# Kernel optimization log

Hardware: AMD Instinct MI355X
Metric: run time of the kernel (lower is better)

## Reference

```python
import jax, jax.numpy as jnp
import numpy as np

B = 65536      # batch
DIM = 32       # flow dimension
NH = 24        # hidden width of each per-dim MLP
PARITY = False # order = reversed(range(dim)) when parity is False
NEG_SLOPE = 0.2


def _causal_mask(dim, dtype):
    # mask[k, j] = 1 if j <= k ; stacked layer k corresponds to torch layer i=k+1
    # which sees x[:, :i] = columns 0..k
    return (jnp.arange(dim)[None, :] <= jnp.arange(dim - 1)[:, None]).astype(dtype)


def setup_inputs() -> dict:
    key = jax.random.key(0)
    ks = jax.random.split(key, 10)
    s = 0.1
    x = jax.random.normal(ks[0], (B, DIM), jnp.float32)
    p0 = jax.random.normal(ks[1], (2,), jnp.float32) * s          # LeafParam(2)
    W1 = jax.random.normal(ks[2], (DIM - 1, NH, DIM), jnp.float32) * s
    W1 = W1 * _causal_mask(DIM, jnp.float32)[:, None, :]          # zero padded cols j > k
    b1 = jax.random.normal(ks[3], (DIM - 1, NH), jnp.float32) * s
    W2 = jax.random.normal(ks[4], (DIM - 1, NH, NH), jnp.float32) * s
    b2 = jax.random.normal(ks[5], (DIM - 1, NH), jnp.float32) * s
    W3 = jax.random.normal(ks[6], (DIM - 1, NH, NH), jnp.float32) * s
    b3 = jax.random.normal(ks[7], (DIM - 1, NH), jnp.float32) * s
    W4 = jax.random.normal(ks[8], (DIM - 1, 2, NH), jnp.float32) * s
    b4 = jax.random.normal(ks[9], (DIM - 1, 2), jnp.float32) * s
    return {"x": x, "p0": p0, "W1": W1, "b1": b1, "W2": W2, "b2": b2,
            "W3": W3, "b3": b3, "W4": W4, "b4": b4}


def reference(x, p0, W1, b1, W2, b2, W3, b3, W4, b4):
    # SlowMAF.forward: per-dim MLP(x[:, :i]) -> (s, t); z[:, order[i]] = x[:, i]*exp(s)+t
    # All dim-1 tiny MLPs are fused into stacked batched GEMMs; the growing slice
    # x[:, :i] is realized via a causal mask on the first-layer weights (same math).
    Bsz, dim = x.shape
    lrelu = lambda h: jnp.where(h > 0, h, NEG_SLOPE * h)  # LeakyReLU(0.2)
    W1m = W1 * _causal_mask(dim, x.dtype)[:, None, :]
    h = lrelu(jnp.einsum('bd,khd->bkh', x, W1m) + b1)      # (B, dim-1, NH)
    h = lrelu(jnp.einsum('bkh,kHh->bkH', h, W2) + b2)
    h = lrelu(jnp.einsum('bkh,kHh->bkH', h, W3) + b3)
    st = jnp.einsum('bkh,koh->bko', h, W4) + b4            # (B, dim-1, 2)
    st0 = jnp.broadcast_to(p0[None, None, :], (Bsz, 1, 2)) # LeafParam for dim 0
    st_all = jnp.concatenate([st0, st], axis=1)            # (B, dim, 2)
    s = st_all[..., 0]
    t = st_all[..., 1]
    vals = x * jnp.exp(s) + t                              # (B, dim)
    order = jnp.arange(dim) if PARITY else jnp.arange(dim)[::-1]
    z = jnp.zeros_like(x).at[:, order].set(vals)
    log_det = jnp.sum(s, axis=1)                           # (B,)
    return z, log_det
```

## Files before the change

kernel.cpp:

```cpp
#include <hip/hip_runtime.h>

#define BATCH 65536
#define DIM 32
#define NEG 0.2f

typedef short    sfrag8 __attribute__((ext_vector_type(8)));
typedef _Float16 hfrag8 __attribute__((ext_vector_type(8)));
typedef _Float16 h2     __attribute__((ext_vector_type(2)));
typedef float    f32x16 __attribute__((ext_vector_type(16)));
typedef unsigned u32x4  __attribute__((ext_vector_type(4)));

__device__ __forceinline__ short f2h(float v) {
    _Float16 h = (_Float16)v;
    return __builtin_bit_cast(short, h);
}

__device__ __forceinline__ h2 cvt2h(float a, float b) {
    return __builtin_bit_cast(h2, __builtin_amdgcn_cvt_pkrtz(a, b));
}

__device__ __forceinline__ unsigned pack2h(float a, float b) {
    return __builtin_bit_cast(unsigned, __builtin_amdgcn_cvt_pkrtz(a, b));
}

__device__ float frag_elem(int k, int f, int r, int h, int j,
    const float* W1, const float* b1, const float* W2, const float* b2,
    const float* W3, const float* b3, const float* W4, const float* b4)
{
    if (f == 0) return (r < 24) ? W1[k*768 + r*32 + 8*h + j] : 0.f;
    if (f == 1) {
        if (r >= 24) return 0.f;
        int c = 16 + 8*h + j;
        if (c == 31) return b1[k*24 + r];
        return W1[k*768 + r*32 + c];
    }
    const float* W; const float* bb; int R;
    if (f < 4)      { W = W2 + k*576; bb = b2 + k*24; R = 24; }
    else if (f < 6) { W = W3 + k*576; bb = b3 + k*24; R = 24; }
    else            { W = W4 + k*48;  bb = b4 + k*2;  R = 2;  }
    if (r >= R) return 0.f;
    if ((f & 1) == 0) {
        int feat = j + 4*h + (j >= 4 ? 4 : 0);
        return W[r*24 + feat];
    } else {
        if (j < 4)            return W[r*24 + 16 + 4*h + j];
        if (j == 4 && h == 0) return bb[r];
        return 0.f;
    }
}

__global__ __launch_bounds__(256) void prep_frags(
    const float* __restrict__ W1, const float* __restrict__ b1,
    const float* __restrict__ W2, const float* __restrict__ b2,
    const float* __restrict__ W3, const float* __restrict__ b3,
    const float* __restrict__ W4, const float* __restrict__ b4,
    short* __restrict__ wsf)
{
    int t = blockIdx.x * 256 + threadIdx.x;
    int lane = t & 63, f = (t >> 6) & 7, k = t >> 9;
    int r = lane & 31, h = lane >> 5;
    sfrag8 o;
    #pragma unroll
    for (int j = 0; j < 8; j++)
        o[j] = f2h(frag_elem(k, f, r, h, j, W1, b1, W2, b2, W3, b3, W4, b4));
    *(sfrag8*)(wsf + (size_t)t * 8) = o;
}

__device__ __forceinline__ void transition(const f32x16 a, unsigned c1,
                                           hfrag8& blo, hfrag8& bhi)
{
    const h2 s02 = {(_Float16)0.2f, (_Float16)0.2f};
    unsigned P[6];
    #pragma unroll
    for (int g = 0; g < 6; g++) {
        h2 v = cvt2h(a[2*g], a[2*g + 1]);
        h2 r = __builtin_elementwise_max(v, v * s02);
        P[g] = __builtin_bit_cast(unsigned, r);
    }
    blo = __builtin_bit_cast(hfrag8, (u32x4){P[0], P[1], P[2], P[3]});
    bhi = __builtin_bit_cast(hfrag8, (u32x4){P[4], P[5], c1, 0u});
}

template<bool PREPPED>
__global__ __launch_bounds__(256, 4) void maf2(
    const float* __restrict__ x, const float* __restrict__ p0,
    const float* __restrict__ W1, const float* __restrict__ b1,
    const float* __restrict__ W2, const float* __restrict__ b2,
    const float* __restrict__ W3, const float* __restrict__ b3,
    const float* __restrict__ W4, const float* __restrict__ b4,
    const short* __restrict__ wsf,
    float* __restrict__ out)
{
    __shared__ short lds_f[4 * 8 * 64 * 8];

    const int  kg   = blockIdx.y;
    const int  lane = threadIdx.x & 63;
    const int  wave = threadIdx.x >> 6;
    const bool hi   = lane >= 32;
    const int  h    = hi ? 1 : 0;
    const int  r    = lane & 31;
    const int  k0   = kg ? 4*kg - 1 : 0;
    const int  nk   = kg ? 4 : 3;
    const int  c0   = 28 - 4*kg;
    const int  col  = (blockIdx.x * 4 + wave) * 32 + r;
    const unsigned c1 = hi ? 0u : 0x3C00u;

    if (PREPPED) {
        const sfrag8* src = (const sfrag8*)(wsf + (size_t)k0 * 4096);
        sfrag8* dst = (sfrag8*)lds_f;
        #pragma unroll
        for (int c = 0; c < 8; c++) {
            int u = c * 256 + threadIdx.x;
            dst[u] = src[u];
        }
        __syncthreads();
    }

    const float* xp = x + (size_t)col * DIM;
    float4 q0 = *(const float4*)(xp + 8*h);
    float4 q1 = *(const float4*)(xp + 8*h + 4);
    float4 q2 = *(const float4*)(xp + 16 + 8*h);
    float4 q3 = *(const float4*)(xp + 16 + 8*h + 4);
    unsigned L0 = pack2h(q0.x, q0.y), L1 = pack2h(q0.z, q0.w);
    unsigned L2 = pack2h(q1.x, q1.y), L3 = pack2h(q1.z, q1.w);
    unsigned H0 = pack2h(q2.x, q2.y), H1 = pack2h(q2.z, q2.w);
    unsigned H2 = pack2h(q3.x, q3.y);
    unsigned H3 = pack2h(q3.z, hi ? 1.0f : q3.w);
    hfrag8 xlo = __builtin_bit_cast(hfrag8, (u32x4){L0, L1, L2, L3});
    hfrag8 xhi = __builtin_bit_cast(hfrag8, (u32x4){H0, H1, H2, H3});

    float4 qa = *(const float4*)(xp + 4*kg);
    float xa[4] = {qa.x, qa.y, qa.z, qa.w};

    f32x16 Z;
    #pragma unroll
    for (int q = 0; q < 16; q++) Z[q] = 0.f;

    float za[4];
    float ld = 0.f;

    #pragma unroll
    for (int i = 0; i < 4; i++) {
        if (i < nk) {
            hfrag8 Fi[8];
            if (!PREPPED) {
                int k = k0 + i;
                #pragma unroll
                for (int f = 0; f < 8; f++)
                    #pragma unroll
                    for (int j = 0; j < 8; j++)
                        Fi[f][j] = (_Float16)frag_elem(k, f, r, h, j,
                                                       W1, b1, W2, b2, W3, b3, W4, b4);
            }
            const short* lf = lds_f + i * 4096;
            #define LDF(ff) (PREPPED ? *(const hfrag8*)(lf + (ff)*512 + lane*8) : Fi[ff])

            f32x16 a1  = __builtin_amdgcn_mfma_f32_32x32x16_f16(LDF(0), xlo, Z, 0, 0, 0);
            f32x16 acc = __builtin_amdgcn_mfma_f32_32x32x16_f16(LDF(1), xhi, a1, 0, 0, 0);
            hfrag8 blo, bh2;
            transition(acc, c1, blo, bh2);
            a1  = __builtin_amdgcn_mfma_f32_32x32x16_f16(LDF(2), blo, Z, 0, 0, 0);
            acc = __builtin_amdgcn_mfma_f32_32x32x16_f16(LDF(3), bh2, a1, 0, 0, 0);
            transition(acc, c1, blo, bh2);
            a1  = __builtin_amdgcn_mfma_f32_32x32x16_f16(LDF(4), blo, Z, 0, 0, 0);
            acc = __builtin_amdgcn_mfma_f32_32x32x16_f16(LDF(5), bh2, a1, 0, 0, 0);
            transition(acc, c1, blo, bh2);
            a1  = __builtin_amdgcn_mfma_f32_32x32x16_f16(LDF(6), blo, Z, 0, 0, 0);
            acc = __builtin_amdgcn_mfma_f32_32x32x16_f16(LDF(7), bh2, a1, 0, 0, 0);
            #undef LDF

            float s  = acc[0];
            float tt = acc[1];
            float e  = __expf(s);
            if (kg) { za[3 - i] = xa[i] * e + tt; }
            else if (i < 3) { za[2 - i] = xa[i + 1] * e + tt; }
            ld += s;
        }
    }

    if (kg == 0) {
        float s0 = p0[0], t0 = p0[1];
        float e0 = __expf(s0);
        za[3] = xa[0] * e0 + t0;
        ld += s0;
    }

    if (!hi) {
        float4 v; v.x = za[0]; v.y = za[1]; v.z = za[2]; v.w = za[3];
        *(float4*)(out + (size_t)col * DIM + c0) = v;
        atomicAdd(out + (size_t)BATCH * DIM + col, ld);
    }
}

extern "C" void kernel_launch(void* const* d_in, const int* in_sizes, int n_in,
                              void* d_out, int out_size, void* d_ws, size_t ws_size,
                              hipStream_t stream)
{
    const float* x  = (const float*)d_in[0];
    const float* p0 = (const float*)d_in[1];
    const float* W1 = (const float*)d_in[2];
    const float* b1 = (const float*)d_in[3];
    const float* W2 = (const float*)d_in[4];
    const float* b2 = (const float*)d_in[5];
    const float* W3 = (const float*)d_in[6];
    const float* b3 = (const float*)d_in[7];
    const float* W4 = (const float*)d_in[8];
    const float* b4 = (const float*)d_in[9];
    float* out = (float*)d_out;

    const size_t FRG = (size_t)31 * 8 * 64 * 8;
    if (ws_size >= FRG * sizeof(short)) {
        short* wsf = (short*)d_ws;
        prep_frags<<<62, 256, 0, stream>>>(W1, b1, W2, b2, W3, b3, W4, b4, wsf);
        maf2<true><<<dim3(512, 8), 256, 0, stream>>>(
            x, p0, W1, b1, W2, b2, W3, b3, W4, b4, wsf, out);
    } else {
        maf2<false><<<dim3(512, 8), 256, 0, stream>>>(
            x, p0, W1, b1, W2, b2, W3, b3, W4, b4, nullptr, out);
    }
}
```

Before: 97.92 us.

## Process all dimension groups per block with LDS-staged x and coalesced output

The 2D grid over (column block, dim group) is collapsed to a 1D grid in which each block loops over all 8 dim groups. Each iteration streams that group's weight fragments into LDS, and x is staged once through swizzled LDS. Outputs are gathered in LDS and written back as coalesced float4s. The log-det sum is accumulated in registers and written directly, which removes the atomicAdd and the eightfold re-reading of x. The cost is a serialized loop with two barriers per group, lower occupancy (launch bounds 2, 64KB LDS), and weight loads that are no longer shared across concurrent blocks.

```diff
diff --git a/kernel.cpp b/kernel.cpp
--- a/kernel.cpp
+++ b/kernel.cpp
@@ -2,7 +2,6 @@
 
 #define BATCH 65536
 #define DIM 32
-#define NEG 0.2f
 
 typedef short    sfrag8 __attribute__((ext_vector_type(8)));
 typedef _Float16 hfrag8 __attribute__((ext_vector_type(8)));
@@ -74,15 +73,15 @@
     #pragma unroll
     for (int g = 0; g < 6; g++) {
         h2 v = cvt2h(a[2*g], a[2*g + 1]);
-        h2 r = __builtin_elementwise_max(v, v * s02);
-        P[g] = __builtin_bit_cast(unsigned, r);
+        h2 rr = __builtin_elementwise_max(v, v * s02);
+        P[g] = __builtin_bit_cast(unsigned, rr);
     }
     blo = __builtin_bit_cast(hfrag8, (u32x4){P[0], P[1], P[2], P[3]});
     bhi = __builtin_bit_cast(hfrag8, (u32x4){P[4], P[5], c1, 0u});
 }
 
 template<bool PREPPED>
-__global__ __launch_bounds__(256, 4) void maf2(
+__global__ __launch_bounds__(256, 2) void maf3(
     const float* __restrict__ x, const float* __restrict__ p0,
     const float* __restrict__ W1, const float* __restrict__ b1,
     const float* __restrict__ W2, const float* __restrict__ b2,
@@ -91,105 +90,132 @@
     const short* __restrict__ wsf,
     float* __restrict__ out)
 {
-    __shared__ short lds_f[4 * 8 * 64 * 8];
-
-    const int  kg   = blockIdx.y;
-    const int  lane = threadIdx.x & 63;
-    const int  wave = threadIdx.x >> 6;
+    __shared__ float4 lds[4096];
+    const int  tid  = threadIdx.x;
+    const int  lane = tid & 63;
+    const int  wave = tid >> 6;
     const bool hi   = lane >= 32;
     const int  h    = hi ? 1 : 0;
     const int  r    = lane & 31;
-    const int  k0   = kg ? 4*kg - 1 : 0;
-    const int  nk   = kg ? 4 : 3;
-    const int  c0   = 28 - 4*kg;
-    const int  col  = (blockIdx.x * 4 + wave) * 32 + r;
+    const int  c    = wave*32 + r;
+    const int  s    = c & 7;
+    const int  colblk = blockIdx.x * 128;
     const unsigned c1 = hi ? 0u : 0x3C00u;
 
-    if (PREPPED) {
-        const sfrag8* src = (const sfrag8*)(wsf + (size_t)k0 * 4096);
-        sfrag8* dst = (sfrag8*)lds_f;
+    {
+        const float4* xg = (const float4*)(x + (size_t)colblk * DIM);
         #pragma unroll
-        for (int c = 0; c < 8; c++) {
-            int u = c * 256 + threadIdx.x;
-            dst[u] = src[u];
-        }
-        __syncthreads();
-    }
-
-    const float* xp = x + (size_t)col * DIM;
-    float4 q0 = *(const float4*)(xp + 8*h);
-    float4 q1 = *(const float4*)(xp + 8*h + 4);
-    float4 q2 = *(const float4*)(xp + 16 + 8*h);
-    float4 q3 = *(const float4*)(xp + 16 + 8*h + 4);
-    unsigned L0 = pack2h(q0.x, q0.y), L1 = pack2h(q0.z, q0.w);
-    unsigned L2 = pack2h(q1.x, q1.y), L3 = pack2h(q1.z, q1.w);
-    unsigned H0 = pack2h(q2.x, q2.y), H1 = pack2h(q2.z, q2.w);
-    unsigned H2 = pack2h(q3.x, q3.y);
-    unsigned H3 = pack2h(q3.z, hi ? 1.0f : q3.w);
-    hfrag8 xlo = __builtin_bit_cast(hfrag8, (u32x4){L0, L1, L2, L3});
-    hfrag8 xhi = __builtin_bit_cast(hfrag8, (u32x4){H0, H1, H2, H3});
-
-    float4 qa = *(const float4*)(xp + 4*kg);
-    float xa[4] = {qa.x, qa.y, qa.z, qa.w};
+        for (int j = 0; j < 4; j++) {
+            int a16 = j * 256 + tid;
+            int cc = a16 >> 3, q = a16 & 7;
+            lds[cc*8 + (q ^ (cc & 7))] = xg[a16];
+        }
+    }
+    __syncthreads();
+
+    hfrag8 xlo, xhi;
+    {
+        float4 q0 = lds[c*8 + ((2*h)     ^ s)];
+        float4 q1 = lds[c*8 + ((2*h + 1) ^ s)];
+        float4 q2 = lds[c*8 + ((4 + 2*h) ^ s)];
+        float4 q3 = lds[c*8 + ((5 + 2*h) ^ s)];
+        unsigned L0 = pack2h(q0.x, q0.y), L1 = pack2h(q0.z, q0.w);
+        unsigned L2 = pack2h(q1.x, q1.y), L3 = pack2h(q1.z, q1.w);
+        unsigned H0 = pack2h(q2.x, q2.y), H1 = pack2h(q2.z, q2.w);
+        unsigned H2 = pack2h(q3.x, q3.y);
+        unsigned H3 = pack2h(q3.z, hi ? 1.0f : q3.w);
+        xlo = __builtin_bit_cast(hfrag8, (u32x4){L0, L1, L2, L3});
+        xhi = __builtin_bit_cast(hfrag8, (u32x4){H0, H1, H2, H3});
+    }
 
     f32x16 Z;
     #pragma unroll
     for (int q = 0; q < 16; q++) Z[q] = 0.f;
-
-    float za[4];
     float ld = 0.f;
-
-    #pragma unroll
-    for (int i = 0; i < 4; i++) {
-        if (i < nk) {
-            hfrag8 Fi[8];
-            if (!PREPPED) {
-                int k = k0 + i;
+    _Float16* flh = (_Float16*)(lds + 1024);
+
+    #pragma unroll 1
+    for (int g = 0; g < 8; g++) {
+        const int k0 = g ? 4*g - 1 : 0;
+
+        __syncthreads();
+        if constexpr (PREPPED) {
+            const float4* src = (const float4*)(wsf) + (size_t)k0 * 512;
+            #pragma unroll
+            for (int c2 = 0; c2 < 8; c2++) {
+                int u = c2 * 256 + tid;
+                lds[1024 + u] = src[u];
+            }
+        } else {
+            const int k = k0 + wave;
+            _Float16* dst = flh + wave*4096 + lane*8;
+            #pragma unroll
+            for (int f = 0; f < 8; f++) {
+                hfrag8 o;
                 #pragma unroll
-                for (int f = 0; f < 8; f++)
-                    #pragma unroll
-                    for (int j = 0; j < 8; j++)
-                        Fi[f][j] = (_Float16)frag_elem(k, f, r, h, j,
-                                                       W1, b1, W2, b2, W3, b3, W4, b4);
+                for (int j = 0; j < 8; j++)
+                    o[j] = (_Float16)frag_elem(k, f, r, h, j,
+                                               W1, b1, W2, b2, W3, b3, W4, b4);
+                *(hfrag8*)(dst + f*512) = o;
             }
-            const short* lf = lds_f + i * 4096;
-            #define LDF(ff) (PREPPED ? *(const hfrag8*)(lf + (ff)*512 + lane*8) : Fi[ff])
-
-            f32x16 a1  = __builtin_amdgcn_mfma_f32_32x32x16_f16(LDF(0), xlo, Z, 0, 0, 0);
-            f32x16 acc = __builtin_amdgcn_mfma_f32_32x32x16_f16(LDF(1), xhi, a1, 0, 0, 0);
-            hfrag8 blo, bh2;
-            transition(acc, c1, blo, bh2);
-            a1  = __builtin_amdgcn_mfma_f32_32x32x16_f16(LDF(2), blo, Z, 0, 0, 0);
-            acc = __builtin_amdgcn_mfma_f32_32x32x16_f16(LDF(3), bh2, a1, 0, 0, 0);
-            transition(acc, c1, blo, bh2);
-            a1  = __builtin_amdgcn_mfma_f32_32x32x16_f16(LDF(4), blo, Z, 0, 0, 0);
-            acc = __builtin_amdgcn_mfma_f32_32x32x16_f16(LDF(5), bh2, a1, 0, 0, 0);
-            transition(acc, c1, blo, bh2);
-            a1  = __builtin_amdgcn_mfma_f32_32x32x16_f16(LDF(6), blo, Z, 0, 0, 0);
-            acc = __builtin_amdgcn_mfma_f32_32x32x16_f16(LDF(7), bh2, a1, 0, 0, 0);
-            #undef LDF
-
-            float s  = acc[0];
-            float tt = acc[1];
-            float e  = __expf(s);
-            if (kg) { za[3 - i] = xa[i] * e + tt; }
-            else if (i < 3) { za[2 - i] = xa[i + 1] * e + tt; }
-            ld += s;
-        }
-    }
-
-    if (kg == 0) {
-        float s0 = p0[0], t0 = p0[1];
-        float e0 = __expf(s0);
-        za[3] = xa[0] * e0 + t0;
-        ld += s0;
-    }
-
-    if (!hi) {
-        float4 v; v.x = za[0]; v.y = za[1]; v.z = za[2]; v.w = za[3];
-        *(float4*)(out + (size_t)col * DIM + c0) = v;
-        atomicAdd(out + (size_t)BATCH * DIM + col, ld);
-    }
+        }
+        __syncthreads();
+
+        float4 qa = lds[c*8 + (g ^ s)];
+        float xa[4] = {qa.x, qa.y, qa.z, qa.w};
+        float za[4];
+
+        #pragma unroll
+        for (int i = 0; i < 4; i++) {
+            if (g || i < 3) {
+                const _Float16* lf = flh + i * 4096;
+                #define LDF(ff) (*(const hfrag8*)(lf + (ff)*512 + lane*8))
+                f32x16 a1  = __builtin_amdgcn_mfma_f32_32x32x16_f16(LDF(0), xlo, Z, 0, 0, 0);
+                f32x16 acc = __builtin_amdgcn_mfma_f32_32x32x16_f16(LDF(1), xhi, a1, 0, 0, 0);
+                hfrag8 blo, bh2;
+                transition(acc, c1, blo, bh2);
+                a1  = __builtin_amdgcn_mfma_f32_32x32x16_f16(LDF(2), blo, Z, 0, 0, 0);
+                acc = __builtin_amdgcn_mfma_f32_32x32x16_f16(LDF(3), bh2, a1, 0, 0, 0);
+                transition(acc, c1, blo, bh2);
+                a1  = __builtin_amdgcn_mfma_f32_32x32x16_f16(LDF(4), blo, Z, 0, 0, 0);
+                acc = __builtin_amdgcn_mfma_f32_32x32x16_f16(LDF(5), bh2, a1, 0, 0, 0);
+                transition(acc, c1, blo, bh2);
+                a1  = __builtin_amdgcn_mfma_f32_32x32x16_f16(LDF(6), blo, Z, 0, 0, 0);
+                acc = __builtin_amdgcn_mfma_f32_32x32x16_f16(LDF(7), bh2, a1, 0, 0, 0);
+                #undef LDF
+                float sv = acc[0], tv = acc[1];
+                float e  = __expf(sv);
+                if (g) za[3 - i] = xa[i] * e + tv;
+                else   za[2 - i] = xa[i + 1] * e + tv;
+                ld += sv;
+            }
+        }
+
+        if (g == 0) {
+            float s0 = p0[0], t0 = p0[1];
+            za[3] = xa[0] * __expf(s0) + t0;
+            ld += s0;
+        }
+
+        if (!hi) {
+            float4 v; v.x = za[0]; v.y = za[1]; v.z = za[2]; v.w = za[3];
+            lds[3072 + c*8 + ((7 - g) ^ s)] = v;
+        }
+    }
+
+    __syncthreads();
+
+    {
+        float4* og = (float4*)out + (size_t)colblk * 8;
+        #pragma unroll
+        for (int j = 0; j < 4; j++) {
+            int a16 = j * 256 + tid;
+            int cc = a16 >> 3, q = a16 & 7;
+            og[a16] = lds[3072 + cc*8 + (q ^ (cc & 7))];
+        }
+    }
+    if (!hi)
+        out[(size_t)BATCH * DIM + colblk + c] = ld;
 }
 
 extern "C" void kernel_launch(void* const* d_in, const int* in_sizes, int n_in,
@@ -212,10 +238,10 @@
     if (ws_size >= FRG * sizeof(short)) {
         short* wsf = (short*)d_ws;
         prep_frags<<<62, 256, 0, stream>>>(W1, b1, W2, b2, W3, b3, W4, b4, wsf);
-        maf2<true><<<dim3(512, 8), 256, 0, stream>>>(
+        maf3<true><<<512, 256, 0, stream>>>(
             x, p0, W1, b1, W2, b2, W3, b3, W4, b4, wsf, out);
     } else {
-        maf2<false><<<dim3(512, 8), 256, 0, stream>>>(
+        maf3<false><<<512, 256, 0, stream>>>(
             x, p0, W1, b1, W2, b2, W3, b3, W4, b4, nullptr, out);
     }
 }
```

New measurement: 98.14 us. No clear change (+0.2%).
